# Kernel tuning notes

Hardware: AMD Instinct MI355X
Metric: run time of the kernel (lower is better)

## Reference

```python
import jax, jax.numpy as jnp
import numpy as np
from jax.scipy.special import logsumexp


def setup_inputs() -> dict:
    key = jax.random.key(0)
    k = jax.random.split(key, 8)
    B, T, K, L = 32, 128, 16, 16
    s = 0.05
    y_batch = jax.random.uniform(k[0], (B, T, 1, 28, 28), dtype=jnp.float32)
    enc_w1 = jax.random.normal(k[1], (400, 784), dtype=jnp.float32) * s
    enc_b1 = jnp.zeros((400,), jnp.float32)
    enc_w2 = jax.random.normal(k[2], (2 * L, 400), dtype=jnp.float32) * s
    enc_b2 = jnp.zeros((2 * L,), jnp.float32)
    dec_fc_w = jax.random.normal(k[3], (400, L + K), dtype=jnp.float32) * s
    dec_fc_b = jnp.zeros((400,), jnp.float32)
    dec_w = jax.random.normal(k[4], (784, 400), dtype=jnp.float32) * s
    dec_b = jnp.zeros((784,), jnp.float32)
    log_pi = jnp.zeros((K,), jnp.float32)
    log_A = jax.random.normal(k[5], (K, K), dtype=jnp.float32)
    log_A = log_A.at[jnp.arange(K), jnp.arange(K)].set(-1e9)  # fill_diagonal_(-1e9)
    eps = jax.random.normal(k[6], (B * T, L), dtype=jnp.float32)
    return dict(y_batch=y_batch, enc_w1=enc_w1, enc_b1=enc_b1, enc_w2=enc_w2,
                enc_b2=enc_b2, dec_fc_w=dec_fc_w, dec_fc_b=dec_fc_b, dec_w=dec_w,
                dec_b=dec_b, log_pi=log_pi, log_A=log_A, eps=eps)


def reference(y_batch, enc_w1, enc_b1, enc_w2, enc_b2, dec_fc_w, dec_fc_b,
              dec_w, dec_b, log_pi, log_A, eps):
    B, T = y_batch.shape[0], y_batch.shape[1]
    K = log_pi.shape[0]
    L = eps.shape[1]
    N = B * T
    # ---- VAE emission log-likelihoods (compute_log_bk); dropout in eval mode ----
    y_flat = y_batch.reshape(N, 784)
    h = jax.nn.relu(y_flat @ enc_w1.T + enc_b1)                 # [N,400]
    ml = h @ enc_w2.T + enc_b2                                   # [N,2L]
    mu, logvar = ml[:, :L], ml[:, L:]
    z = mu + eps * jnp.exp(0.5 * logvar)                         # reparameterize
    # decode(z, one_hot(k)) for all k at once: split cat-linear into z part + k column
    Wz, Wx = dec_fc_w[:, :L], dec_fc_w[:, L:]                    # [400,L],[400,K]
    base = z @ Wz.T + dec_fc_b                                   # [N,400]
    hk = jax.nn.relu(base[None, :, :] + Wx.T[:, None, :])        # [K,N,400]
    y_rec = jax.nn.sigmoid(jnp.einsum('knh,oh->kno', hk, dec_w) + dec_b)  # [K,N,784]
    # binary_cross_entropy with torch's log clamp at -100
    logp = jnp.clip(jnp.log(y_rec), -100.0, None)
    log1mp = jnp.clip(jnp.log(1.0 - y_rec), -100.0, None)
    bce = -(y_flat[None] * logp + (1.0 - y_flat[None]) * log1mp)  # [K,N,784]
    recon = bce.sum(-1) / 100.0                                   # [K,N]
    log_bk = (-recon).reshape(K, B, T).transpose(1, 2, 0)         # [B,T,K]
    # ---- forward-backward in log domain ----
    lp = jnp.log(jax.nn.softmax(log_pi) + 1e-9)
    lA = jnp.log(jax.nn.softmax(log_A, axis=1) + 1e-9)
    lb_rest = jnp.moveaxis(log_bk[:, 1:], 1, 0)                   # [T-1,B,K]
    a0 = lp + log_bk[:, 0]                                        # [B,K]

    def fstep(prev, lb_t):
        cur = logsumexp(prev[:, :, None] + lA[None], axis=1) + lb_t
        return cur, cur

    _, alphas = jax.lax.scan(fstep, a0, lb_rest)
    log_alpha = jnp.concatenate([a0[:, None], jnp.moveaxis(alphas, 0, 1)], axis=1)  # [B,T,K]

    bT = jnp.zeros((B, K), log_bk.dtype)

    def bstep(nxt, lb_t1):
        cur = logsumexp(lA[None] + (lb_t1 + nxt)[:, None, :], axis=2)
        return cur, cur

    _, betas = jax.lax.scan(bstep, bT, lb_rest, reverse=True)     # betas[t] = beta_t, t=0..T-2
    log_beta = jnp.concatenate([jnp.moveaxis(betas, 0, 1), bT[:, None]], axis=1)  # [B,T,K]

    lg = log_alpha + log_beta
    log_gamma = lg - logsumexp(lg, axis=2, keepdims=True)

    lxi = (log_alpha[:, :-1, :, None] + lA[None, None]
           + (log_bk[:, 1:] + log_beta[:, 1:])[:, :, None, :])    # [B,T-1,K,K]
    lxi = lxi - logsumexp(lxi, axis=(2, 3), keepdims=True)
    return jnp.exp(log_gamma), jnp.exp(lxi)
```

## Files before the change

kernel.cpp:

```cpp
#include <hip/hip_runtime.h>
#include <math.h>


typedef _Float16 h8v __attribute__((ext_vector_type(8)));
typedef _Float16 h4v __attribute__((ext_vector_type(4)));
typedef float f16v __attribute__((ext_vector_type(16)));

__global__ __launch_bounds__(256)
void k_prep(const float* __restrict__ dw, const float* __restrict__ ew1,
            _Float16* __restrict__ dwh, _Float16* __restrict__ w1h) {
  int idx = blockIdx.x * 256 + threadIdx.x;
  if (idx < 896 * 448) {
    int o = idx / 448, h2 = idx - o * 448;
    float v = (o < 784 && h2 < 400) ? dw[o * 400 + h2] : 0.f;
    dwh[idx] = (_Float16)v;
  } else if (idx < 896 * 448 + 512 * 800) {
    int j = idx - 896 * 448;
    int i = j / 800, kc = j - i * 800;
    float v = (i < 400 && kc < 784) ? ew1[i * 784 + kc] : 0.f;
    w1h[j] = (_Float16)v;
  }
}

#define E1ST 40
__global__ __launch_bounds__(256, 2)
void k_enc1(const float* __restrict__ y, const _Float16* __restrict__ w1h,
            const float* __restrict__ b1, float* __restrict__ hout) {
  __shared__ __align__(16) _Float16 Ah[64 * E1ST];
  __shared__ __align__(16) _Float16 Bh[128 * E1ST];
  const int tid = threadIdx.x;
  const int i0 = blockIdx.x * 128;
  const int n0 = blockIdx.y * 64;
  const int wav = tid >> 6, lane = tid & 63;
  const int wn = wav >> 1, wi = wav & 1;
  const int ln = lane & 31, kg = lane >> 5;

  f16v acc[2];
#pragma unroll
  for (int j = 0; j < 2; ++j)
#pragma unroll
    for (int r = 0; r < 16; ++r) acc[j][r] = 0.f;

  const int ar = tid >> 3, ac4 = (tid & 7) * 4;
  const int br = tid >> 2, bg = (tid & 3) * 8;

#pragma unroll 1
  for (int hc = 0; hc < 25; ++hc) {
    const int h0 = hc * 32;
    __syncthreads();
#pragma unroll
    for (int it = 0; it < 2; ++it) {
      int r = ar + 32 * it;
      float4 a = make_float4(0.f, 0.f, 0.f, 0.f);
      if (h0 + ac4 < 784) a = *(const float4*)&y[(n0 + r) * 784 + h0 + ac4];
      h4v hv;
      hv[0] = (_Float16)a.x; hv[1] = (_Float16)a.y;
      hv[2] = (_Float16)a.z; hv[3] = (_Float16)a.w;
      *(h4v*)&Ah[r * E1ST + ac4] = hv;
    }
#pragma unroll
    for (int it = 0; it < 2; ++it) {
      int r = br + 64 * it;
      *(h8v*)&Bh[r * E1ST + bg] = *(const h8v*)&w1h[(i0 + r) * 800 + h0 + bg];
    }
    __syncthreads();
#pragma unroll
    for (int kk = 0; kk < 2; ++kk) {
      const int ko = kk * 16 + kg * 8;
      h8v a  = *(const h8v*)&Ah[(wn * 32 + ln) * E1ST + ko];
      h8v b0 = *(const h8v*)&Bh[(wi * 64 + ln) * E1ST + ko];
      h8v b1 = *(const h8v*)&Bh[(wi * 64 + 32 + ln) * E1ST + ko];
      acc[0] = __builtin_amdgcn_mfma_f32_32x32x16_f16(a, b0, acc[0], 0, 0, 0);
      acc[1] = __builtin_amdgcn_mfma_f32_32x32x16_f16(a, b1, acc[1], 0, 0, 0);
    }
  }
#pragma unroll
  for (int j = 0; j < 2; ++j) {
    const int i = i0 + wi * 64 + j * 32 + ln;
    if (i < 400) {
      const float bias = b1[i];
#pragma unroll
      for (int reg = 0; reg < 16; ++reg) {
        const int row = n0 + wn * 32 + (reg & 3) + 8 * (reg >> 2) + 4 * kg;
        hout[row * 400 + i] = fmaxf(acc[j][reg] + bias, 0.f);
      }
    }
  }
}

__global__ __launch_bounds__(128, 4)
void k_enc2z(const float* __restrict__ h, const float* __restrict__ w2,
             const float* __restrict__ b2, const float* __restrict__ eps,
             float* __restrict__ z) {
  __shared__ __align__(16) float h_lds[4 * 400];
  __shared__ __align__(16) float w2_lds[32 * 404];
  __shared__ float ml_lds[4 * 32];
  const int tid = threadIdx.x;
  const int n0 = blockIdx.x * 4;
  for (int idx = tid; idx < 400; idx += 128) {
    int r = idx / 100, c = idx % 100;
    *(float4*)&h_lds[r * 400 + c * 4] = *(const float4*)&h[(n0 + r) * 400 + c * 4];
  }
  for (int idx = tid; idx < 3200; idx += 128) {
    int r = idx / 100, c = idx % 100;
    *(float4*)&w2_lds[r * 404 + c * 4] = *(const float4*)&w2[r * 400 + c * 4];
  }
  __syncthreads();
  const int c_ = tid & 31, n_ = tid >> 5;
  float acc = 0.f;
  for (int q = 0; q < 100; ++q) {
    float4 hv = *(const float4*)&h_lds[n_ * 400 + q * 4];
    float4 wv = *(const float4*)&w2_lds[c_ * 404 + q * 4];
    acc += hv.x * wv.x + hv.y * wv.y + hv.z * wv.z + hv.w * wv.w;
  }
  ml_lds[n_ * 32 + c_] = acc + b2[c_];
  __syncthreads();
  if (tid < 64) {
    int n2 = tid >> 4, l = tid & 15;
    float mu = ml_lds[n2 * 32 + l];
    float lv = ml_lds[n2 * 32 + 16 + l];
    z[(n0 + n2) * 16 + l] = mu + eps[(n0 + n2) * 16 + l] * expf(0.5f * lv);
  }
}

__global__ __launch_bounds__(256, 4)
void k_base(const float* __restrict__ z, const float* __restrict__ dfw,
            const float* __restrict__ dfb, float* __restrict__ basep) {
  __shared__ float z_lds[16 * 16];
  __shared__ __align__(16) float wz_lds[400 * 20];
  const int tid = threadIdx.x;
  const int n0 = blockIdx.x * 16;
  if (tid < 64) {
    int n = tid >> 2, c = (tid & 3) * 4;
    *(float4*)&z_lds[n * 16 + c] = *(const float4*)&z[(n0 + n) * 16 + c];
  }
  for (int idx = tid; idx < 1600; idx += 256) {
    int i = idx >> 2, c = (idx & 3) * 4;
    *(float4*)&wz_lds[i * 20 + c] = *(const float4*)&dfw[i * 32 + c];
  }
  __syncthreads();
  for (int idx = tid; idx < 7168; idx += 256) {
    int n = idx / 448, i = idx - n * 448;
    float acc = 0.f;
    if (i < 400) {
      acc = dfb[i];
#pragma unroll
      for (int q = 0; q < 4; ++q) {
        float4 zv = *(const float4*)&z_lds[n * 16 + q * 4];
        float4 wv = *(const float4*)&wz_lds[i * 20 + q * 4];
        acc += zv.x * wv.x + zv.y * wv.y + zv.z * wv.z + zv.w * wv.w;
      }
    }
    basep[(n0 + n) * 448 + i] = acc;
  }
}

#define DST 72
__global__ __launch_bounds__(256, 2)
void k_dec(const float* __restrict__ basep, const float* __restrict__ dfw,
           const _Float16* __restrict__ dwh, const float* __restrict__ decb,
           const float* __restrict__ y, float* __restrict__ lb) {
  __shared__ __align__(16) _Float16 Ah[128 * DST];
  __shared__ __align__(16) _Float16 Bh[128 * DST];
  __shared__ float wx[448];
  __shared__ float red[256];

  const int tid = threadIdx.x;
  const int k = blockIdx.x;
  const int n0 = blockIdx.y * 128;
  const int wav = tid >> 6, lane = tid & 63;
  const int wn = wav >> 1, wo = wav & 1;
  const int ln = lane & 31, kg = lane >> 5;

  for (int i = tid; i < 448; i += 256) wx[i] = (i < 400) ? dfw[i * 32 + 16 + k] : 0.f;

  float pr[2][16];
#pragma unroll
  for (int i = 0; i < 2; ++i)
#pragma unroll
    for (int r = 0; r < 16; ++r) pr[i][r] = 0.f;

  const int ar = tid >> 4, ac4 = (tid & 15) * 4;
  const int br = tid >> 3, bg = (tid & 7) * 8;
  const float* aptr = basep + (long)(n0 + ar) * 448 + ac4;

  float4 apf[8];
#pragma unroll
  for (int it = 0; it < 8; ++it) apf[it] = *(const float4*)&aptr[(16 * it) * 448];

#pragma unroll 1
  for (int ot = 0; ot < 7; ++ot) {
    const int o0 = ot * 128;
    const bool full = (ot < 6);
    f16v acc[2][2];
#pragma unroll
    for (int i = 0; i < 2; ++i)
#pragma unroll
      for (int j = 0; j < 2; ++j)
#pragma unroll
        for (int r = 0; r < 16; ++r) acc[i][j][r] = 0.f;

#pragma unroll 1
    for (int hc = 0; hc < 7; ++hc) {
      const int h0 = hc * 64;
      h8v bpf[4];
#pragma unroll
      for (int it = 0; it < 4; ++it)
        bpf[it] = *(const h8v*)&dwh[(o0 + br + 32 * it) * 448 + h0 + bg];
      __syncthreads();
      {
        float4 w = *(const float4*)&wx[h0 + ac4];
#pragma unroll
        for (int it = 0; it < 8; ++it) {
          int r = ar + 16 * it;
          h4v hv;
          hv[0] = (_Float16)fmaxf(apf[it].x + w.x, 0.f);
          hv[1] = (_Float16)fmaxf(apf[it].y + w.y, 0.f);
          hv[2] = (_Float16)fmaxf(apf[it].z + w.z, 0.f);
          hv[3] = (_Float16)fmaxf(apf[it].w + w.w, 0.f);
          *(h4v*)&Ah[r * DST + ac4] = hv;
        }
      }
#pragma unroll
      for (int it = 0; it < 4; ++it)
        *(h8v*)&Bh[(br + 32 * it) * DST + bg] = bpf[it];
      __syncthreads();
      if (!(ot == 6 && hc == 6)) {
        const int hn = (hc == 6) ? 0 : (hc + 1) * 64;
#pragma unroll
        for (int it = 0; it < 8; ++it)
          apf[it] = *(const float4*)&aptr[(16 * it) * 448 + hn];
      }
#pragma unroll
      for (int kk = 0; kk < 4; ++kk) {
        const int ko = kk * 16 + kg * 8;
        h8v a0 = *(const h8v*)&Ah[(wn * 64 + ln) * DST + ko];
        h8v a1 = *(const h8v*)&Ah[(wn * 64 + 32 + ln) * DST + ko];
        h8v b0 = *(const h8v*)&Bh[(wo * 64 + ln) * DST + ko];
        h8v b1 = *(const h8v*)&Bh[(wo * 64 + 32 + ln) * DST + ko];
        if (full) {
          acc[0][0] = __builtin_amdgcn_mfma_f32_32x32x16_f16(a0, b0, acc[0][0], 0, 0, 0);
          acc[1][0] = __builtin_amdgcn_mfma_f32_32x32x16_f16(a1, b0, acc[1][0], 0, 0, 0);
          acc[0][1] = __builtin_amdgcn_mfma_f32_32x32x16_f16(a0, b1, acc[0][1], 0, 0, 0);
          acc[1][1] = __builtin_amdgcn_mfma_f32_32x32x16_f16(a1, b1, acc[1][1], 0, 0, 0);
        } else if (wo == 0) {
          acc[0][0] = __builtin_amdgcn_mfma_f32_32x32x16_f16(a0, b0, acc[0][0], 0, 0, 0);
          acc[1][0] = __builtin_amdgcn_mfma_f32_32x32x16_f16(a1, b0, acc[1][0], 0, 0, 0);
        }
      }
    }
#pragma unroll
    for (int j = 0; j < 2; ++j) {
      const int o = o0 + wo * 64 + j * 32 + ln;
      const bool valid = (o < 784);
      const float bias = valid ? decb[o] : 0.f;
#pragma unroll
      for (int i = 0; i < 2; ++i) {
        if (valid) {
#pragma unroll
          for (int reg = 0; reg < 16; ++reg) {
            const int row = wn * 64 + i * 32 + (reg & 3) + 8 * (reg >> 2) + 4 * kg;
            float x = acc[i][j][reg] + bias;
            float yv = y[(n0 + row) * 784 + o];
            float spx = fmaxf(x, 0.f) + __logf(1.f + __expf(-fabsf(x)));
            float t2 = fminf(spx, 100.f);
            float t1 = fminf(spx - x, 100.f);
            pr[i][reg] += t2 + yv * (t1 - t2);
          }
        }
      }
    }
  }
#pragma unroll
  for (int i = 0; i < 2; ++i)
#pragma unroll
    for (int reg = 0; reg < 16; ++reg) {
      float v = pr[i][reg];
      v += __shfl_xor(v, 1, 64);
      v += __shfl_xor(v, 2, 64);
      v += __shfl_xor(v, 4, 64);
      v += __shfl_xor(v, 8, 64);
      v += __shfl_xor(v, 16, 64);
      if (ln == 0) {
        const int row = wn * 64 + i * 32 + (reg & 3) + 8 * (reg >> 2) + 4 * kg;
        red[wo * 128 + row] = v;
      }
    }
  __syncthreads();
  if (tid < 128) {
    float s = red[tid] + red[128 + tid];
    lb[(n0 + tid) * 16 + k] = -(s / 100.0f);
  }
}

__global__ __launch_bounds__(256, 2)
void k_hmm(const float* __restrict__ lb, const float* __restrict__ lpi,
           const float* __restrict__ lA, float* __restrict__ out,
           float* __restrict__ g_ah, float* __restrict__ g_pb,
           float* __restrict__ g_sinv, float* __restrict__ g_Al) {
  __shared__ float btl[128 * 16];
  __shared__ float ah[128 * 16];
  __shared__ float bh[128 * 16];
  __shared__ float braw[128 * 16];
  __shared__ float A_l[16 * 17];
  __shared__ float pi_l[16];
  const int tid = threadIdx.x;
  const int b = blockIdx.x;

  for (int idx = tid; idx < 512; idx += 256)
    *(float4*)&btl[idx * 4] = *(const float4*)&lb[b * 2048 + idx * 4];
  if (tid < 16) {
    const int j = tid;
    float m = -1e30f;
#pragma unroll
    for (int q = 0; q < 16; ++q) m = fmaxf(m, lA[j * 16 + q]);
    float e[16]; float s = 0.f;
#pragma unroll
    for (int q = 0; q < 16; ++q) { e[q] = expf(lA[j * 16 + q] - m); s += e[q]; }
    float inv = 1.f / s;
#pragma unroll
    for (int q = 0; q < 16; ++q) {
      float v = e[q] * inv + 1e-9f;
      A_l[j * 17 + q] = v;
      g_Al[j * 16 + q] = v;
    }
  } else if (tid == 16) {
    float m = -1e30f;
#pragma unroll
    for (int q = 0; q < 16; ++q) m = fmaxf(m, lpi[q]);
    float e[16]; float s = 0.f;
#pragma unroll
    for (int q = 0; q < 16; ++q) { e[q] = expf(lpi[q] - m); s += e[q]; }
    float inv = 1.f / s;
#pragma unroll
    for (int q = 0; q < 16; ++q) pi_l[q] = e[q] * inv + 1e-9f;
  }
  __syncthreads();
  if (tid < 128) {
    const int t = tid;
    float v[16]; float m = -1e30f;
#pragma unroll
    for (int q = 0; q < 16; ++q) { v[q] = btl[t * 16 + q]; m = fmaxf(m, v[q]); }
#pragma unroll
    for (int q = 0; q < 16; ++q) btl[t * 16 + q] = expf(v[q] - m);
  }
  __syncthreads();
  const int lane = tid & 63;
  const int kk = lane & 15, grp = lane >> 4;
  if (tid < 64) {
    float v0 = pi_l[kk] * btl[kk];
    float ss0 = v0;
    ss0 += __shfl_xor(ss0, 1, 64); ss0 += __shfl_xor(ss0, 2, 64);
    ss0 += __shfl_xor(ss0, 4, 64); ss0 += __shfl_xor(ss0, 8, 64);
    if (grp == 0) ah[kk] = v0 / ss0;
    for (int t = 1; t < 128; ++t) {
      float acc = 0.f;
#pragma unroll
      for (int jj = 0; jj < 4; ++jj) {
        int j = grp * 4 + jj;
        acc = fmaf(ah[(t - 1) * 16 + j], A_l[j * 17 + kk], acc);
      }
      acc += __shfl_xor(acc, 16, 64);
      acc += __shfl_xor(acc, 32, 64);
      float v = acc * btl[t * 16 + kk];
      float ss = v;
      ss += __shfl_xor(ss, 1, 64); ss += __shfl_xor(ss, 2, 64);
      ss += __shfl_xor(ss, 4, 64); ss += __shfl_xor(ss, 8, 64);
      if (grp == 0) ah[t * 16 + kk] = v / ss;
    }
  } else if (tid < 128) {
    if (grp == 0) bh[127 * 16 + kk] = 1.f;
    for (int t = 126; t >= 0; --t) {
      float acc = 0.f;
#pragma unroll
      for (int q = 0; q < 4; ++q) {
        int k2 = grp * 4 + q;
        acc = fmaf(A_l[kk * 17 + k2], btl[(t + 1) * 16 + k2] * bh[(t + 1) * 16 + k2], acc);
      }
      acc += __shfl_xor(acc, 16, 64);
      acc += __shfl_xor(acc, 32, 64);
      float ss = acc;
      ss += __shfl_xor(ss, 1, 64); ss += __shfl_xor(ss, 2, 64);
      ss += __shfl_xor(ss, 4, 64); ss += __shfl_xor(ss, 8, 64);
      if (grp == 0) { braw[t * 16 + kk] = acc; bh[t * 16 + kk] = acc / ss; }
    }
  }
  __syncthreads();
  if (tid < 128) {
    const int t = tid;
    float g[16]; float s2 = 0.f;
#pragma unroll
    for (int q = 0; q < 16; ++q) { g[q] = ah[t * 16 + q] * bh[t * 16 + q]; s2 += g[q]; }
    float inv = 1.f / s2;
#pragma unroll
    for (int c = 0; c < 4; ++c) {
      float4 o;
      o.x = g[c * 4 + 0] * inv; o.y = g[c * 4 + 1] * inv;
      o.z = g[c * 4 + 2] * inv; o.w = g[c * 4 + 3] * inv;
      *(float4*)&out[(b * 128 + t) * 16 + c * 4] = o;
      float4 av = *(float4*)&ah[t * 16 + c * 4];
      *(float4*)&g_ah[(b * 128 + t) * 16 + c * 4] = av;
      float4 p;
      p.x = btl[t * 16 + c * 4 + 0] * bh[t * 16 + c * 4 + 0];
      p.y = btl[t * 16 + c * 4 + 1] * bh[t * 16 + c * 4 + 1];
      p.z = btl[t * 16 + c * 4 + 2] * bh[t * 16 + c * 4 + 2];
      p.w = btl[t * 16 + c * 4 + 3] * bh[t * 16 + c * 4 + 3];
      *(float4*)&g_pb[(b * 128 + t) * 16 + c * 4] = p;
    }
  } else {
    const int t = tid - 128;
    if (t < 127) {
      float s2 = 0.f;
#pragma unroll
      for (int q = 0; q < 16; ++q) s2 += ah[t * 16 + q] * braw[t * 16 + q];
      g_sinv[b * 128 + t] = 1.f / s2;
    }
  }
}

__global__ __launch_bounds__(256)
void k_xi(const float* __restrict__ g_ah, const float* __restrict__ g_pb,
          const float* __restrict__ g_sinv, const float* __restrict__ g_Al,
          float* __restrict__ out) {
  const int b = blockIdx.x, t = blockIdx.y;
  const int tid = threadIdx.x;
  const int j = tid >> 4, k2 = tid & 15;
  float val = g_ah[(b * 128 + t) * 16 + j] * g_Al[j * 16 + k2] *
              g_pb[(b * 128 + t + 1) * 16 + k2] * g_sinv[b * 128 + t];
  out[65536 + (b * 127 + t) * 256 + tid] = val;
}

extern "C" void kernel_launch(void* const* d_in, const int* in_sizes, int n_in,
                              void* d_out, int out_size, void* d_ws, size_t ws_size,
                              hipStream_t stream) {
  (void)in_sizes; (void)n_in; (void)out_size; (void)ws_size;
  const float* y   = (const float*)d_in[0];
  const float* ew1 = (const float*)d_in[1];
  const float* eb1 = (const float*)d_in[2];
  const float* ew2 = (const float*)d_in[3];
  const float* eb2 = (const float*)d_in[4];
  const float* dfw = (const float*)d_in[5];
  const float* dfb = (const float*)d_in[6];
  const float* dw  = (const float*)d_in[7];
  const float* db  = (const float*)d_in[8];
  const float* lpi = (const float*)d_in[9];
  const float* lA  = (const float*)d_in[10];
  const float* eps = (const float*)d_in[11];
  float* out = (float*)d_out;

  float* ws = (float*)d_ws;
  float* h      = ws;
  float* basep  = ws;
  float* z      = ws + 1835008;
  float* lb     = z + 65536;
  _Float16* dwh = (_Float16*)(lb + 65536);
  _Float16* w1h = dwh + 896 * 448;
  float* g_ah   = (float*)(w1h + 512 * 800);
  float* g_pb   = g_ah + 65536;
  float* g_sinv = g_pb + 65536;
  float* g_Al   = g_sinv + 4096;

  k_prep<<<3168, 256, 0, stream>>>(dw, ew1, dwh, w1h);
  k_enc1<<<dim3(4, 64), 256, 0, stream>>>(y, w1h, eb1, h);
  k_enc2z<<<1024, 128, 0, stream>>>(h, ew2, eb2, eps, z);
  k_base<<<256, 256, 0, stream>>>(z, dfw, dfb, basep);
  k_dec<<<dim3(16, 32), 256, 0, stream>>>(basep, dfw, dwh, db, y, lb);
  k_hmm<<<32, 256, 0, stream>>>(lb, lpi, lA, out, g_ah, g_pb, g_sinv, g_Al);
  k_xi<<<dim3(32, 127), 256, 0, stream>>>(g_ah, g_pb, g_sinv, g_Al, out);
}
```

Baseline: 335.3 us.

## Split decoder output tiles across blocks and reduce BCE sums with atomics

The decoder kernel previously looped over all seven output-column tiles inside one block (512 blocks). Now each block handles a single (row tile, state, output tile) triple, giving 3584 blocks with an XCD-aware index swizzle and a higher occupancy hint. Per-block partial BCE sums are combined with atomicAdd into a buffer zeroed in the prep kernel, and the -1/100 scaling moves into the HMM load. This raises parallelism and occupancy at the cost of recomputing the A-tile relu conversion per output tile, atomic traffic, and nondeterministic summation order.

```diff
diff --git a/kernel.cpp b/kernel.cpp
--- a/kernel.cpp
+++ b/kernel.cpp
@@ -8,8 +8,10 @@
 
 __global__ __launch_bounds__(256)
 void k_prep(const float* __restrict__ dw, const float* __restrict__ ew1,
-            _Float16* __restrict__ dwh, _Float16* __restrict__ w1h) {
+            _Float16* __restrict__ dwh, _Float16* __restrict__ w1h,
+            float* __restrict__ lb) {
   int idx = blockIdx.x * 256 + threadIdx.x;
+  if (idx < 65536) lb[idx] = 0.f;
   if (idx < 896 * 448) {
     int o = idx / 448, h2 = idx - o * 448;
     float v = (o < 784 && h2 < 400) ? dw[o * 400 + h2] : 0.f;
@@ -156,7 +158,7 @@
 }
 
 #define DST 72
-__global__ __launch_bounds__(256, 2)
+__global__ __launch_bounds__(256, 4)
 void k_dec(const float* __restrict__ basep, const float* __restrict__ dfw,
            const _Float16* __restrict__ dwh, const float* __restrict__ decb,
            const float* __restrict__ y, float* __restrict__ lb) {
@@ -166,20 +168,22 @@
   __shared__ float red[256];
 
   const int tid = threadIdx.x;
-  const int k = blockIdx.x;
-  const int n0 = blockIdx.y * 128;
+  const int id  = blockIdx.x;
+  const int lin = (id & 7) * 448 + (id >> 3);
+  const int n_i = lin / 112;
+  const int rem = lin - n_i * 112;
+  const int k   = rem / 7;
+  const int ot  = rem - k * 7;
+  const int n0  = n_i * 128;
+  const int o0  = ot * 128;
+  const bool full = (ot < 6);
+
   const int wav = tid >> 6, lane = tid & 63;
   const int wn = wav >> 1, wo = wav & 1;
   const int ln = lane & 31, kg = lane >> 5;
 
   for (int i = tid; i < 448; i += 256) wx[i] = (i < 400) ? dfw[i * 32 + 16 + k] : 0.f;
 
-  float pr[2][16];
-#pragma unroll
-  for (int i = 0; i < 2; ++i)
-#pragma unroll
-    for (int r = 0; r < 16; ++r) pr[i][r] = 0.f;
-
   const int ar = tid >> 4, ac4 = (tid & 15) * 4;
   const int br = tid >> 3, bg = (tid & 7) * 8;
   const float* aptr = basep + (long)(n0 + ar) * 448 + ac4;
@@ -188,108 +192,96 @@
 #pragma unroll
   for (int it = 0; it < 8; ++it) apf[it] = *(const float4*)&aptr[(16 * it) * 448];
 
+  f16v acc[2][2];
+#pragma unroll
+  for (int i = 0; i < 2; ++i)
+#pragma unroll
+    for (int j = 0; j < 2; ++j)
+#pragma unroll
+      for (int r = 0; r < 16; ++r) acc[i][j][r] = 0.f;
+
 #pragma unroll 1
-  for (int ot = 0; ot < 7; ++ot) {
-    const int o0 = ot * 128;
-    const bool full = (ot < 6);
-    f16v acc[2][2];
-#pragma unroll
-    for (int i = 0; i < 2; ++i)
-#pragma unroll
-      for (int j = 0; j < 2; ++j)
-#pragma unroll
-        for (int r = 0; r < 16; ++r) acc[i][j][r] = 0.f;
-
-#pragma unroll 1
-    for (int hc = 0; hc < 7; ++hc) {
-      const int h0 = hc * 64;
-      h8v bpf[4];
-#pragma unroll
-      for (int it = 0; it < 4; ++it)
-        bpf[it] = *(const h8v*)&dwh[(o0 + br + 32 * it) * 448 + h0 + bg];
-      __syncthreads();
-      {
-        float4 w = *(const float4*)&wx[h0 + ac4];
-#pragma unroll
-        for (int it = 0; it < 8; ++it) {
-          int r = ar + 16 * it;
-          h4v hv;
-          hv[0] = (_Float16)fmaxf(apf[it].x + w.x, 0.f);
-          hv[1] = (_Float16)fmaxf(apf[it].y + w.y, 0.f);
-          hv[2] = (_Float16)fmaxf(apf[it].z + w.z, 0.f);
-          hv[3] = (_Float16)fmaxf(apf[it].w + w.w, 0.f);
-          *(h4v*)&Ah[r * DST + ac4] = hv;
+  for (int hc = 0; hc < 7; ++hc) {
+    const int h0 = hc * 64;
+    h8v bpf[4];
+#pragma unroll
+    for (int it = 0; it < 4; ++it)
+      bpf[it] = *(const h8v*)&dwh[(o0 + br + 32 * it) * 448 + h0 + bg];
+    __syncthreads();
+    {
+      float4 w = *(const float4*)&wx[h0 + ac4];
+#pragma unroll
+      for (int it = 0; it < 8; ++it) {
+        int r = ar + 16 * it;
+        h4v hv;
+        hv[0] = (_Float16)fmaxf(apf[it].x + w.x, 0.f);
+        hv[1] = (_Float16)fmaxf(apf[it].y + w.y, 0.f);
+        hv[2] = (_Float16)fmaxf(apf[it].z + w.z, 0.f);
+        hv[3] = (_Float16)fmaxf(apf[it].w + w.w, 0.f);
+        *(h4v*)&Ah[r * DST + ac4] = hv;
+      }
+    }
+#pragma unroll
+    for (int it = 0; it < 4; ++it)
+      *(h8v*)&Bh[(br + 32 * it) * DST + bg] = bpf[it];
+    __syncthreads();
+    if (hc < 6) {
+      const int hn = (hc + 1) * 64;
+#pragma unroll
+      for (int it = 0; it < 8; ++it)
+        apf[it] = *(const float4*)&aptr[(16 * it) * 448 + hn];
+    }
+#pragma unroll
+    for (int kk = 0; kk < 4; ++kk) {
+      const int ko = kk * 16 + kg * 8;
+      h8v a0 = *(const h8v*)&Ah[(wn * 64 + ln) * DST + ko];
+      h8v a1 = *(const h8v*)&Ah[(wn * 64 + 32 + ln) * DST + ko];
+      h8v b0 = *(const h8v*)&Bh[(wo * 64 + ln) * DST + ko];
+      h8v b1 = *(const h8v*)&Bh[(wo * 64 + 32 + ln) * DST + ko];
+      if (full) {
+        acc[0][0] = __builtin_amdgcn_mfma_f32_32x32x16_f16(a0, b0, acc[0][0], 0, 0, 0);
+        acc[1][0] = __builtin_amdgcn_mfma_f32_32x32x16_f16(a1, b0, acc[1][0], 0, 0, 0);
+        acc[0][1] = __builtin_amdgcn_mfma_f32_32x32x16_f16(a0, b1, acc[0][1], 0, 0, 0);
+        acc[1][1] = __builtin_amdgcn_mfma_f32_32x32x16_f16(a1, b1, acc[1][1], 0, 0, 0);
+      } else if (wo == 0) {
+        acc[0][0] = __builtin_amdgcn_mfma_f32_32x32x16_f16(a0, b0, acc[0][0], 0, 0, 0);
+        acc[1][0] = __builtin_amdgcn_mfma_f32_32x32x16_f16(a1, b0, acc[1][0], 0, 0, 0);
+      }
+    }
+  }
+  const int obase = o0 + wo * 64;
+  const float bj0 = (obase + ln < 784) ? decb[obase + ln] : 0.f;
+  const float bj1 = (obase + 32 + ln < 784) ? decb[obase + 32 + ln] : 0.f;
+#pragma unroll
+  for (int i = 0; i < 2; ++i) {
+#pragma unroll
+    for (int reg = 0; reg < 16; ++reg) {
+      const int row = wn * 64 + i * 32 + (reg & 3) + 8 * (reg >> 2) + 4 * kg;
+      float v = 0.f;
+#pragma unroll
+      for (int j = 0; j < 2; ++j) {
+        const int o = obase + j * 32 + ln;
+        if (o < 784) {
+          float x = acc[i][j][reg] + (j ? bj1 : bj0);
+          float yv = y[(n0 + row) * 784 + o];
+          float spx = fmaxf(x, 0.f) + __logf(1.f + __expf(-fabsf(x)));
+          float t2 = fminf(spx, 100.f);
+          float t1 = fminf(spx - x, 100.f);
+          v += t2 + yv * (t1 - t2);
         }
       }
-#pragma unroll
-      for (int it = 0; it < 4; ++it)
-        *(h8v*)&Bh[(br + 32 * it) * DST + bg] = bpf[it];
-      __syncthreads();
-      if (!(ot == 6 && hc == 6)) {
-        const int hn = (hc == 6) ? 0 : (hc + 1) * 64;
-#pragma unroll
-        for (int it = 0; it < 8; ++it)
-          apf[it] = *(const float4*)&aptr[(16 * it) * 448 + hn];
-      }
-#pragma unroll
-      for (int kk = 0; kk < 4; ++kk) {
-        const int ko = kk * 16 + kg * 8;
-        h8v a0 = *(const h8v*)&Ah[(wn * 64 + ln) * DST + ko];
-        h8v a1 = *(const h8v*)&Ah[(wn * 64 + 32 + ln) * DST + ko];
-        h8v b0 = *(const h8v*)&Bh[(wo * 64 + ln) * DST + ko];
-        h8v b1 = *(const h8v*)&Bh[(wo * 64 + 32 + ln) * DST + ko];
-        if (full) {
-          acc[0][0] = __builtin_amdgcn_mfma_f32_32x32x16_f16(a0, b0, acc[0][0], 0, 0, 0);
-          acc[1][0] = __builtin_amdgcn_mfma_f32_32x32x16_f16(a1, b0, acc[1][0], 0, 0, 0);
-          acc[0][1] = __builtin_amdgcn_mfma_f32_32x32x16_f16(a0, b1, acc[0][1], 0, 0, 0);
-          acc[1][1] = __builtin_amdgcn_mfma_f32_32x32x16_f16(a1, b1, acc[1][1], 0, 0, 0);
-        } else if (wo == 0) {
-          acc[0][0] = __builtin_amdgcn_mfma_f32_32x32x16_f16(a0, b0, acc[0][0], 0, 0, 0);
-          acc[1][0] = __builtin_amdgcn_mfma_f32_32x32x16_f16(a1, b0, acc[1][0], 0, 0, 0);
-        }
-      }
-    }
-#pragma unroll
-    for (int j = 0; j < 2; ++j) {
-      const int o = o0 + wo * 64 + j * 32 + ln;
-      const bool valid = (o < 784);
-      const float bias = valid ? decb[o] : 0.f;
-#pragma unroll
-      for (int i = 0; i < 2; ++i) {
-        if (valid) {
-#pragma unroll
-          for (int reg = 0; reg < 16; ++reg) {
-            const int row = wn * 64 + i * 32 + (reg & 3) + 8 * (reg >> 2) + 4 * kg;
-            float x = acc[i][j][reg] + bias;
-            float yv = y[(n0 + row) * 784 + o];
-            float spx = fmaxf(x, 0.f) + __logf(1.f + __expf(-fabsf(x)));
-            float t2 = fminf(spx, 100.f);
-            float t1 = fminf(spx - x, 100.f);
-            pr[i][reg] += t2 + yv * (t1 - t2);
-          }
-        }
-      }
-    }
-  }
-#pragma unroll
-  for (int i = 0; i < 2; ++i)
-#pragma unroll
-    for (int reg = 0; reg < 16; ++reg) {
-      float v = pr[i][reg];
       v += __shfl_xor(v, 1, 64);
       v += __shfl_xor(v, 2, 64);
       v += __shfl_xor(v, 4, 64);
       v += __shfl_xor(v, 8, 64);
       v += __shfl_xor(v, 16, 64);
-      if (ln == 0) {
-        const int row = wn * 64 + i * 32 + (reg & 3) + 8 * (reg >> 2) + 4 * kg;
-        red[wo * 128 + row] = v;
-      }
-    }
+      if (ln == 0) red[wo * 128 + row] = v;
+    }
+  }
   __syncthreads();
   if (tid < 128) {
     float s = red[tid] + red[128 + tid];
-    lb[(n0 + tid) * 16 + k] = -(s / 100.0f);
+    atomicAdd(&lb[(n0 + tid) * 16 + k], s);
   }
 }
 
@@ -307,8 +299,11 @@
   const int tid = threadIdx.x;
   const int b = blockIdx.x;
 
-  for (int idx = tid; idx < 512; idx += 256)
-    *(float4*)&btl[idx * 4] = *(const float4*)&lb[b * 2048 + idx * 4];
+  for (int idx = tid; idx < 512; idx += 256) {
+    float4 v = *(const float4*)&lb[b * 2048 + idx * 4];
+    v.x *= -0.01f; v.y *= -0.01f; v.z *= -0.01f; v.w *= -0.01f;
+    *(float4*)&btl[idx * 4] = v;
+  }
   if (tid < 16) {
     const int j = tid;
     float m = -1e30f;
@@ -460,11 +455,11 @@
   float* g_sinv = g_pb + 65536;
   float* g_Al   = g_sinv + 4096;
 
-  k_prep<<<3168, 256, 0, stream>>>(dw, ew1, dwh, w1h);
+  k_prep<<<3168, 256, 0, stream>>>(dw, ew1, dwh, w1h, lb);
   k_enc1<<<dim3(4, 64), 256, 0, stream>>>(y, w1h, eb1, h);
   k_enc2z<<<1024, 128, 0, stream>>>(h, ew2, eb2, eps, z);
   k_base<<<256, 256, 0, stream>>>(z, dfw, dfb, basep);
-  k_dec<<<dim3(16, 32), 256, 0, stream>>>(basep, dfw, dwh, db, y, lb);
+  k_dec<<<3584, 256, 0, stream>>>(basep, dfw, dwh, db, y, lb);
   k_hmm<<<32, 256, 0, stream>>>(lb, lpi, lA, out, g_ah, g_pb, g_sinv, g_Al);
   k_xi<<<dim3(32, 127), 256, 0, stream>>>(g_ah, g_pb, g_sinv, g_Al, out);
 }
```

After: 932.3 us. 178% more time.
